# Kernel tuning notes

Measured on AMD Instinct MI355X. Metric: run time of the kernel, lower is better.

The kernel has to match this reference:

```python
import jax, jax.numpy as jnp
import numpy as np

# Sampled-block sizes (fanouts [25, 10], batch of 1024 seeds)
N_SRC1, N_DST1, N_E1 = 292864, 11264, 281600
N_DST2, N_E2 = 1024, 10240
IN, H, C = 256, 256, 47


def setup_inputs() -> dict:
    key = jax.random.key(0)
    ks = jax.random.split(key, 9)
    s_in = 1.0 / np.sqrt(IN)
    s_h = 1.0 / np.sqrt(H)
    x = jax.random.normal(ks[0], (N_SRC1, IN), jnp.float32)
    src1 = jax.random.randint(ks[1], (N_E1,), 0, N_SRC1)
    dst1 = jnp.sort(jax.random.randint(ks[2], (N_E1,), 0, N_DST1))
    src2 = jax.random.randint(ks[3], (N_E2,), 0, N_DST1)
    dst2 = jnp.sort(jax.random.randint(ks[4], (N_E2,), 0, N_DST2))
    return dict(
        x=x, src1=src1, dst1=dst1, src2=src2, dst2=dst2,
        W_self1=jax.random.normal(ks[5], (IN, H), jnp.float32) * s_in,
        W_neigh1=jax.random.normal(ks[6], (IN, H), jnp.float32) * s_in,
        b1=jnp.zeros((H,), jnp.float32),
        W_self2=jax.random.normal(ks[7], (H, C), jnp.float32) * s_h,
        W_neigh2=jax.random.normal(ks[8], (H, C), jnp.float32) * s_h,
        b2=jnp.zeros((C,), jnp.float32),
    )


def _sage_mean(h_src, src, dst, n_dst, W_self, W_neigh, b):
    # DGL SAGEConv(mean): out = fc_self(h_dst) + fc_neigh(mean_{neighbors} h_src) + b
    gathered = h_src[src]                                   # [E, F] gather
    agg = jax.ops.segment_sum(gathered, dst, num_segments=n_dst)
    deg = jax.ops.segment_sum(jnp.ones((src.shape[0],), h_src.dtype), dst,
                              num_segments=n_dst)
    h_neigh = agg / jnp.maximum(deg, 1.0)[:, None]          # mean aggregation
    h_dst = h_src[:n_dst]                                   # dst nodes are prefix of src
    return h_dst @ W_self + h_neigh @ W_neigh + b


def reference(x, src1, dst1, src2, dst2,
              W_self1, W_neigh1, b1, W_self2, W_neigh2, b2):
    h = _sage_mean(x, src1, dst1, N_DST1, W_self1, W_neigh1, b1)
    h = jax.nn.relu(h)  # dropout is identity in eval mode
    out = _sage_mean(h, src2, dst2, N_DST2, W_self2, W_neigh2, b2)
    return out
```

## Files before the change

### kernel.cpp

```cpp
#include <hip/hip_runtime.h>

#define NSRC1 292864
#define NDST1 11264
#define NE1   281600
#define NDST2 1024
#define NE2   10240

typedef __bf16 bf16x8 __attribute__((ext_vector_type(8)));
typedef float  f32x4  __attribute__((ext_vector_type(4)));

__device__ __forceinline__ unsigned short f2bf(float f) {
    union { float f; unsigned u; } v; v.f = f;
    unsigned r = v.u + 0x7FFF + ((v.u >> 16) & 1);
    return (unsigned short)(r >> 16);
}

__global__ __launch_bounds__(256) void agg1_fused_kernel(
    const float* __restrict__ x,
    const int*   __restrict__ src_idx,
    const int*   __restrict__ dst_idx,
    unsigned short* __restrict__ Abf)
{
    const int lane = threadIdx.x & 63;
    const int w    = threadIdx.x >> 6;
    const int d    = blockIdx.x * 4 + w;

    int lo = 0, hi = NE1;
    while (lo < hi) { int mid = (lo + hi) >> 1; if (dst_idx[mid] <  d) lo = mid + 1; else hi = mid; }
    const int start = lo;
    hi = NE1;
    while (lo < hi) { int mid = (lo + hi) >> 1; if (dst_idx[mid] <= d) lo = mid + 1; else hi = mid; }
    const int end = lo;

    float4 acc = make_float4(0.f, 0.f, 0.f, 0.f);
    for (int e = start; e < end; ++e) {
        const int s = src_idx[e];
        const float4 v = ((const float4*)(x + (size_t)s * 256))[lane];
        acc.x += v.x; acc.y += v.y; acc.z += v.z; acc.w += v.w;
    }
    const int deg = end - start;
    const float inv = 1.0f / (deg > 0 ? (float)deg : 1.0f);

    ushort4 nb;
    nb.x = f2bf(acc.x * inv); nb.y = f2bf(acc.y * inv);
    nb.z = f2bf(acc.z * inv); nb.w = f2bf(acc.w * inv);
    *(ushort4*)(Abf + (size_t)d * 512 + 256 + lane * 4) = nb;

    const float4 xv = ((const float4*)(x + (size_t)d * 256))[lane];
    ushort4 sf;
    sf.x = f2bf(xv.x); sf.y = f2bf(xv.y); sf.z = f2bf(xv.z); sf.w = f2bf(xv.w);
    *(ushort4*)(Abf + (size_t)d * 512 + lane * 4) = sf;
}

__global__ __launch_bounds__(256) void prep_wt_kernel(
    const float* __restrict__ Ws, const float* __restrict__ Wn,
    unsigned short* __restrict__ Wt)
{
    __shared__ float t[64][65];
    const int kb = blockIdx.x * 64, nb = blockIdx.y * 64;
    const float* __restrict__ W = (kb < 256) ? Ws : Wn;
    const int kofs = (kb < 256) ? kb : kb - 256;
    const int c  = threadIdx.x & 63;
    const int r0 = threadIdx.x >> 6;
    #pragma unroll
    for (int i = 0; i < 16; ++i) {
        const int r = r0 + i * 4;
        t[r][c] = W[(size_t)(kofs + r) * 256 + nb + c];
    }
    __syncthreads();
    #pragma unroll
    for (int i = 0; i < 16; ++i) {
        const int r = r0 + i * 4;
        Wt[(size_t)(nb + r) * 512 + kb + c] = f2bf(t[c][r]);
    }
}

#define LDT 40

__global__ __launch_bounds__(256) void gemm1_mfma_kernel(
    const unsigned short* __restrict__ Abf,
    const unsigned short* __restrict__ Wt,
    const float* __restrict__ bias,
    float* __restrict__ h)
{
    __shared__ unsigned short As[128][LDT];
    __shared__ unsigned short Bs[64][LDT];

    const int tid  = threadIdx.x;
    const int lane = tid & 63;
    const int w    = tid >> 6;
    const int wm   = (w & 1) * 64;
    const int wn   = (w >> 1) * 32;
    const int mblk = blockIdx.x * 128;
    const int nblk = blockIdx.y * 64;

    const int r16 = lane & 15;
    const int k0  = (lane >> 4) * 8;

    f32x4 acc[4][2] = {};

    for (int kt = 0; kt < 512; kt += 32) {
        #pragma unroll
        for (int i = 0; i < 2; ++i) {
            const int idx = tid + i * 256;
            const int r  = idx >> 2;
            const int kk = (idx & 3) * 8;
            *(uint4*)&As[r][kk] =
                *(const uint4*)(Abf + (size_t)(mblk + r) * 512 + kt + kk);
        }
        {
            const int r  = tid >> 2;
            const int kk = (tid & 3) * 8;
            *(uint4*)&Bs[r][kk] =
                *(const uint4*)(Wt + (size_t)(nblk + r) * 512 + kt + kk);
        }
        __syncthreads();

        bf16x8 bfrag[2];
        #pragma unroll
        for (int ni = 0; ni < 2; ++ni)
            bfrag[ni] = *(const bf16x8*)&Bs[wn + ni * 16 + r16][k0];
        #pragma unroll
        for (int mi = 0; mi < 4; ++mi) {
            const bf16x8 afrag = *(const bf16x8*)&As[wm + mi * 16 + r16][k0];
            #pragma unroll
            for (int ni = 0; ni < 2; ++ni)
                acc[mi][ni] = __builtin_amdgcn_mfma_f32_16x16x32_bf16(
                    afrag, bfrag[ni], acc[mi][ni], 0, 0, 0);
        }
        __syncthreads();
    }

    #pragma unroll
    for (int mi = 0; mi < 4; ++mi) {
        #pragma unroll
        for (int ni = 0; ni < 2; ++ni) {
            const int col = nblk + wn + ni * 16 + r16;
            const float bb = bias[col];
            #pragma unroll
            for (int r = 0; r < 4; ++r) {
                const int row = mblk + wm + mi * 16 + (lane >> 4) * 4 + r;
                const float v = acc[mi][ni][r] + bb;
                h[(size_t)row * 256 + col] = v > 0.f ? v : 0.f;
            }
        }
    }
}

__global__ __launch_bounds__(64) void agg2_kernel(
    const float* __restrict__ feat,
    const int*   __restrict__ src_idx,
    const int*   __restrict__ dst_idx,
    float* __restrict__ out)
{
    const int d = blockIdx.x;
    int lo = 0, hi = NE2;
    while (lo < hi) { int mid = (lo + hi) >> 1; if (dst_idx[mid] <  d) lo = mid + 1; else hi = mid; }
    const int start = lo;
    hi = NE2;
    while (lo < hi) { int mid = (lo + hi) >> 1; if (dst_idx[mid] <= d) lo = mid + 1; else hi = mid; }
    const int end = lo;

    const int c4 = threadIdx.x;
    float4 acc = make_float4(0.f, 0.f, 0.f, 0.f);
    for (int e = start; e < end; ++e) {
        const int s = src_idx[e];
        const float4 v = ((const float4*)(feat + (size_t)s * 256))[c4];
        acc.x += v.x; acc.y += v.y; acc.z += v.z; acc.w += v.w;
    }
    const int deg = end - start;
    const float inv = 1.0f / (deg > 0 ? (float)deg : 1.0f);
    acc.x *= inv; acc.y *= inv; acc.z *= inv; acc.w *= inv;
    ((float4*)(out + (size_t)d * 256))[c4] = acc;
}

__global__ __launch_bounds__(64) void out_kernel(
    const float* __restrict__ h,
    const float* __restrict__ hn2,
    const float* __restrict__ Ws,
    const float* __restrict__ Wn,
    const float* __restrict__ b,
    float* __restrict__ out)
{
    const int m = blockIdx.x;
    const int c = threadIdx.x;
    if (c >= 47) return;
    float acc = b[c];
    const float* __restrict__ hrow  = h   + (size_t)m * 256;
    const float* __restrict__ hnrow = hn2 + (size_t)m * 256;
    for (int k = 0; k < 256; ++k) {
        acc += hrow[k] * Ws[k * 47 + c] + hnrow[k] * Wn[k * 47 + c];
    }
    out[(size_t)m * 47 + c] = acc;
}

extern "C" void kernel_launch(void* const* d_in, const int* in_sizes, int n_in,
                              void* d_out, int out_size, void* d_ws, size_t ws_size,
                              hipStream_t stream) {
    const float* x    = (const float*)d_in[0];
    const int*   src1 = (const int*)  d_in[1];
    const int*   dst1 = (const int*)  d_in[2];
    const int*   src2 = (const int*)  d_in[3];
    const int*   dst2 = (const int*)  d_in[4];
    const float* Ws1  = (const float*)d_in[5];
    const float* Wn1  = (const float*)d_in[6];
    const float* b1   = (const float*)d_in[7];
    const float* Ws2  = (const float*)d_in[8];
    const float* Wn2  = (const float*)d_in[9];
    const float* b2   = (const float*)d_in[10];
    float* out = (float*)d_out;

    char* ws = (char*)d_ws;
    const size_t sz_Abf = (size_t)NDST1 * 512 * sizeof(unsigned short);
    const size_t sz_h   = (size_t)NDST1 * 256 * sizeof(float);
    const size_t sz_hn2 = (size_t)NDST2 * 256 * sizeof(float);
    unsigned short* Abf = (unsigned short*)(ws);
    float*          h   = (float*)(ws + sz_Abf);
    float*          hn2 = (float*)(ws + sz_Abf + sz_h);
    unsigned short* Wt  = (unsigned short*)(ws + sz_Abf + sz_h + sz_hn2);

    dim3 gw(8, 4);
    prep_wt_kernel<<<gw, 256, 0, stream>>>(Ws1, Wn1, Wt);
    agg1_fused_kernel<<<NDST1 / 4, 256, 0, stream>>>(x, src1, dst1, Abf);
    dim3 g1(NDST1 / 128, 256 / 64);
    gemm1_mfma_kernel<<<g1, 256, 0, stream>>>(Abf, Wt, b1, h);
    agg2_kernel<<<NDST2, 64, 0, stream>>>(h, src2, dst2, hn2);
    out_kernel<<<NDST2, 64, 0, stream>>>(h, hn2, Ws2, Wn2, b2, out);
}
```

Before: 483.4 us.

## Build CSR row pointers once and unroll gather loops with multiple accumulators

Adds a kernel that turns the sorted dst arrays into CSR row-pointer arrays. This replaces the two binary searches each wave ran over the edge list in both aggregation kernels. The gather loops are unrolled by four with independent accumulators so more loads are in flight at once. agg2 and out_kernel now pack four rows per 256-thread block instead of one row per 64-thread block. The cost is one extra kernel launch and a scattered write pass over the row-pointer array.

```diff
diff --git a/kernel.cpp b/kernel.cpp
--- a/kernel.cpp
+++ b/kernel.cpp
@@ -15,35 +15,72 @@
     return (unsigned short)(r >> 16);
 }
 
+__global__ __launch_bounds__(256) void rowptr_kernel(
+    const int* __restrict__ dst1, const int* __restrict__ dst2,
+    int* __restrict__ rp1, int* __restrict__ rp2)
+{
+    const int t = blockIdx.x * 256 + threadIdx.x;
+    if (t < NE1) {
+        const int d  = dst1[t];
+        const int dp = (t == 0) ? -1 : dst1[t - 1];
+        for (int j = dp + 1; j <= d; ++j) rp1[j] = t;
+        if (t == NE1 - 1) for (int j = d + 1; j <= NDST1; ++j) rp1[j] = NE1;
+    } else if (t - NE1 < NE2) {
+        const int e  = t - NE1;
+        const int d  = dst2[e];
+        const int dp = (e == 0) ? -1 : dst2[e - 1];
+        for (int j = dp + 1; j <= d; ++j) rp2[j] = e;
+        if (e == NE2 - 1) for (int j = d + 1; j <= NDST2; ++j) rp2[j] = NE2;
+    }
+}
+
 __global__ __launch_bounds__(256) void agg1_fused_kernel(
     const float* __restrict__ x,
     const int*   __restrict__ src_idx,
-    const int*   __restrict__ dst_idx,
+    const int*   __restrict__ rowptr,
     unsigned short* __restrict__ Abf)
 {
     const int lane = threadIdx.x & 63;
     const int w    = threadIdx.x >> 6;
     const int d    = blockIdx.x * 4 + w;
 
-    int lo = 0, hi = NE1;
-    while (lo < hi) { int mid = (lo + hi) >> 1; if (dst_idx[mid] <  d) lo = mid + 1; else hi = mid; }
-    const int start = lo;
-    hi = NE1;
-    while (lo < hi) { int mid = (lo + hi) >> 1; if (dst_idx[mid] <= d) lo = mid + 1; else hi = mid; }
-    const int end = lo;
-
-    float4 acc = make_float4(0.f, 0.f, 0.f, 0.f);
-    for (int e = start; e < end; ++e) {
+    const int start = rowptr[d];
+    const int end   = rowptr[d + 1];
+
+    float4 a0 = make_float4(0.f,0.f,0.f,0.f);
+    float4 a1 = a0, a2 = a0, a3 = a0;
+
+    int e = start;
+    for (; e + 4 <= end; e += 4) {
+        const int s0 = src_idx[e + 0];
+        const int s1 = src_idx[e + 1];
+        const int s2 = src_idx[e + 2];
+        const int s3 = src_idx[e + 3];
+        const float4 v0 = ((const float4*)(x + (size_t)s0 * 256))[lane];
+        const float4 v1 = ((const float4*)(x + (size_t)s1 * 256))[lane];
+        const float4 v2 = ((const float4*)(x + (size_t)s2 * 256))[lane];
+        const float4 v3 = ((const float4*)(x + (size_t)s3 * 256))[lane];
+        a0.x += v0.x; a0.y += v0.y; a0.z += v0.z; a0.w += v0.w;
+        a1.x += v1.x; a1.y += v1.y; a1.z += v1.z; a1.w += v1.w;
+        a2.x += v2.x; a2.y += v2.y; a2.z += v2.z; a2.w += v2.w;
+        a3.x += v3.x; a3.y += v3.y; a3.z += v3.z; a3.w += v3.w;
+    }
+    for (; e < end; ++e) {
         const int s = src_idx[e];
         const float4 v = ((const float4*)(x + (size_t)s * 256))[lane];
-        acc.x += v.x; acc.y += v.y; acc.z += v.z; acc.w += v.w;
-    }
+        a0.x += v.x; a0.y += v.y; a0.z += v.z; a0.w += v.w;
+    }
+    a0.x += a1.x + a2.x + a3.x;
+    a0.y += a1.y + a2.y + a3.y;
+    a0.z += a1.z + a2.z + a3.z;
+    a0.w += a1.w + a2.w + a3.w;
+
     const int deg = end - start;
     const float inv = 1.0f / (deg > 0 ? (float)deg : 1.0f);
 
     ushort4 nb;
-    nb.x = f2bf(acc.x * inv); nb.y = f2bf(acc.y * inv);
-    nb.z = f2bf(acc.z * inv); nb.w = f2bf(acc.w * inv);
+    nb.x = f2bf(a0.x * inv); nb.y = f2bf(a0.y * inv);
+    nb.z = f2bf(a0.z * inv); nb.w = f2bf(a0.w * inv);
     *(ushort4*)(Abf + (size_t)d * 512 + 256 + lane * 4) = nb;
 
     const float4 xv = ((const float4*)(x + (size_t)d * 256))[lane];
@@ -147,34 +184,54 @@
     }
 }
 
-__global__ __launch_bounds__(64) void agg2_kernel(
+__global__ __launch_bounds__(256) void agg2_kernel(
     const float* __restrict__ feat,
     const int*   __restrict__ src_idx,
-    const int*   __restrict__ dst_idx,
+    const int*   __restrict__ rowptr,
     float* __restrict__ out)
 {
-    const int d = blockIdx.x;
-    int lo = 0, hi = NE2;
-    while (lo < hi) { int mid = (lo + hi) >> 1; if (dst_idx[mid] <  d) lo = mid + 1; else hi = mid; }
-    const int start = lo;
-    hi = NE2;
-    while (lo < hi) { int mid = (lo + hi) >> 1; if (dst_idx[mid] <= d) lo = mid + 1; else hi = mid; }
-    const int end = lo;
-
-    const int c4 = threadIdx.x;
-    float4 acc = make_float4(0.f, 0.f, 0.f, 0.f);
-    for (int e = start; e < end; ++e) {
+    const int lane = threadIdx.x & 63;
+    const int w    = threadIdx.x >> 6;
+    const int d    = blockIdx.x * 4 + w;
+
+    const int start = rowptr[d];
+    const int end   = rowptr[d + 1];
+
+    float4 a0 = make_float4(0.f,0.f,0.f,0.f);
+    float4 a1 = a0, a2 = a0, a3 = a0;
+
+    int e = start;
+    for (; e + 4 <= end; e += 4) {
+        const int s0 = src_idx[e + 0];
+        const int s1 = src_idx[e + 1];
+        const int s2 = src_idx[e + 2];
+        const int s3 = src_idx[e + 3];
+        const float4 v0 = ((const float4*)(feat + (size_t)s0 * 256))[lane];
+        const float4 v1 = ((const float4*)(feat + (size_t)s1 * 256))[lane];
+        const float4 v2 = ((const float4*)(feat + (size_t)s2 * 256))[lane];
+        const float4 v3 = ((const float4*)(feat + (size_t)s3 * 256))[lane];
+        a0.x += v0.x; a0.y += v0.y; a0.z += v0.z; a0.w += v0.w;
+        a1.x += v1.x; a1.y += v1.y; a1.z += v1.z; a1.w += v1.w;
+        a2.x += v2.x; a2.y += v2.y; a2.z += v2.z; a2.w += v2.w;
+        a3.x += v3.x; a3.y += v3.y; a3.z += v3.z; a3.w += v3.w;
+    }
+    for (; e < end; ++e) {
         const int s = src_idx[e];
-        const float4 v = ((const float4*)(feat + (size_t)s * 256))[c4];
-        acc.x += v.x; acc.y += v.y; acc.z += v.z; acc.w += v.w;
-    }
+        const float4 v = ((const float4*)(feat + (size_t)s * 256))[lane];
+        a0.x += v.x; a0.y += v.y; a0.z += v.z; a0.w += v.w;
+    }
+    a0.x += a1.x + a2.x + a3.x;
+    a0.y += a1.y + a2.y + a3.y;
+    a0.z += a1.z + a2.z + a3.z;
+    a0.w += a1.w + a2.w + a3.w;
+
     const int deg = end - start;
     const float inv = 1.0f / (deg > 0 ? (float)deg : 1.0f);
-    acc.x *= inv; acc.y *= inv; acc.z *= inv; acc.w *= inv;
-    ((float4*)(out + (size_t)d * 256))[c4] = acc;
-}
-
-__global__ __launch_bounds__(64) void out_kernel(
+    a0.x *= inv; a0.y *= inv; a0.z *= inv; a0.w *= inv;
+    ((float4*)(out + (size_t)d * 256))[lane] = a0;
+}
+
+__global__ __launch_bounds__(256) void out_kernel(
     const float* __restrict__ h,
     const float* __restrict__ hn2,
     const float* __restrict__ Ws,
@@ -182,12 +239,14 @@
     const float* __restrict__ b,
     float* __restrict__ out)
 {
-    const int m = blockIdx.x;
-    const int c = threadIdx.x;
+    const int w = threadIdx.x >> 6;
+    const int c = threadIdx.x & 63;
+    const int m = blockIdx.x * 4 + w;
     if (c >= 47) return;
     float acc = b[c];
     const float* __restrict__ hrow  = h   + (size_t)m * 256;
     const float* __restrict__ hnrow = hn2 + (size_t)m * 256;
+    #pragma unroll 4
     for (int k = 0; k < 256; ++k) {
         acc += hrow[k] * Ws[k * 47 + c] + hnrow[k] * Wn[k * 47 + c];
     }
@@ -214,16 +273,21 @@
     const size_t sz_Abf = (size_t)NDST1 * 512 * sizeof(unsigned short);
     const size_t sz_h   = (size_t)NDST1 * 256 * sizeof(float);
     const size_t sz_hn2 = (size_t)NDST2 * 256 * sizeof(float);
+    const size_t sz_Wt  = (size_t)256 * 512 * sizeof(unsigned short);
+    const size_t sz_rp1 = (size_t)(NDST1 + 2) * sizeof(int);
     unsigned short* Abf = (unsigned short*)(ws);
     float*          h   = (float*)(ws + sz_Abf);
     float*          hn2 = (float*)(ws + sz_Abf + sz_h);
     unsigned short* Wt  = (unsigned short*)(ws + sz_Abf + sz_h + sz_hn2);
-
+    int*            rp1 = (int*)(ws + sz_Abf + sz_h + sz_hn2 + sz_Wt);
+    int*            rp2 = (int*)(ws + sz_Abf + sz_h + sz_hn2 + sz_Wt + sz_rp1);
+
+    rowptr_kernel<<<(NE1 + NE2 + 255) / 256, 256, 0, stream>>>(dst1, dst2, rp1, rp2);
     dim3 gw(8, 4);
     prep_wt_kernel<<<gw, 256, 0, stream>>>(Ws1, Wn1, Wt);
-    agg1_fused_kernel<<<NDST1 / 4, 256, 0, stream>>>(x, src1, dst1, Abf);
+    agg1_fused_kernel<<<NDST1 / 4, 256, 0, stream>>>(x, src1, rp1, Abf);
     dim3 g1(NDST1 / 128, 256 / 64);
     gemm1_mfma_kernel<<<g1, 256, 0, stream>>>(Abf, Wt, b1, h);
-    agg2_kernel<<<NDST2, 64, 0, stream>>>(h, src2, dst2, hn2);
-    out_kernel<<<NDST2, 64, 0, stream>>>(h, hn2, Ws2, Wn2, b2, out);
-}
+    agg2_kernel<<<NDST2 / 4, 256, 0, stream>>>(h, src2, rp2, hn2);
+    out_kernel<<<NDST2 / 4, 256, 0, stream>>>(h, hn2, Ws2, Wn2, b2, out);
+}
```

After: 451.9 us. -6.5%, faster.
